# Kernel tuning notes

Hardware: AMD Instinct MI355X
Metric: run time of the kernel (lower is better)

The kernel has to match this reference:

```python
import jax, jax.numpy as jnp
import numpy as np
from jax import lax

B = 32
ITERS = 100
ALPHA = 0.3  # keras LeakyReLU default alpha
BN_SCALE = np.float32(1.0 / np.sqrt(1.0 + 1e-3))  # inference BN, default moving stats (mean 0, var 1)


def _make_psf_mat():
    # Gaussian PSF mapping 5184 fine (72x72) code positions -> 81 coarse (9x9) pixels, mat shape (5184, 81)
    sigma = (150.0 / 100.0) * 9.0 / 64.0
    coarse = np.arange(9) + 0.5
    fine = (np.arange(72) + 0.5) * 9.0 / 72.0
    g = np.exp(-(fine[:, None] - coarse[None, :]) ** 2 / (2.0 * sigma ** 2))  # (72, 9)
    mat = np.einsum('ia,jb->ijab', g, g).reshape(5184, 81)
    mat = mat / np.linalg.norm(mat, ord=2)  # spectral-normalize so FISTA (mu=1) is stable
    return mat.astype(np.float32)


def leaky(x):
    return jnp.where(x >= 0, x, ALPHA * x)


def conv(x, k, strides=(1, 1)):
    return lax.conv_general_dilated(x, k, strides, 'SAME',
                                    dimension_numbers=('NHWC', 'HWIO', 'NHWC'))


def _forward(inp, mat, w1_k, w1_b, x1_k, x1_b, c51_k, c51_b, c15_k, c15_b,
             c55_k, c55_b, x2_k, x2_b, y17_k, y17_b, y71_k, y71_b, yc_k, yc_b,
             d1_k, d2_k, h1_w, h1_b, h2_w, h2_b, h3_w, h3_b):
    b = inp.shape[0]
    # w branch
    w = leaky(conv(inp, w1_k) + w1_b)  # (B,9,9,1)
    # z branch -> lambda parameter
    z = inp * BN_SCALE
    z = leaky(conv(z, d1_k, strides=(3, 3)) * BN_SCALE)  # (B,3,3,12), downsample: conv no-bias + BN + LeakyReLU
    z = leaky(conv(z, d2_k, strides=(3, 3)) * BN_SCALE)  # (B,1,1,24)
    z = z.reshape(b, -1)
    z = z @ h1_w + h1_b
    z = z @ h2_w + h2_b
    z = z @ h3_w + h3_b  # (B,1)
    param = 0.1 * jax.nn.sigmoid(z)  # (B,1)
    # x branch: normalize (max of |x| over axis 1 only, as in source)
    x = inp / (0.001 + jnp.max(jnp.abs(inp), axis=1, keepdims=True))
    x = leaky(conv(x, x1_k) + x1_b)  # (B,9,9,3)
    # --- CompressedSensing: 100-iter FISTA, vectorized over batch and 3 channels ---
    im = x.reshape(b, 81, 3).transpose(0, 2, 1)  # (B,3,81) row-major flatten per channel
    lam = (param * 0.1)[:, :, None]  # (B,1,1), mu = 1.0

    def step(carry, _):
        y_tmp, y_last, t = carry
        resid = im - jnp.einsum('bcn,nk->bck', y_tmp, mat)      # (B,3,81)  = im - mat^T y
        re = jnp.einsum('bck,nk->bcn', resid, mat)              # (B,3,5184) = mat (im - mat^T y)
        wv = y_tmp + re
        y_new = jax.nn.relu(wv - lam) - jax.nn.relu(-wv - lam)  # soft threshold
        t_n = (1.0 + jnp.sqrt(1.0 + 4.0 * t * t)) / 2.0
        y_next = y_new + (t - 1.0) / t_n * (y_new - y_last)
        return (y_next, y_new, t_n), None

    init = (jnp.zeros((b, 3, 5184), jnp.float32),
            jnp.zeros((b, 3, 5184), jnp.float32),
            jnp.float32(1.0))
    (_, y_new, _), _ = lax.scan(step, init, None, length=ITERS)
    cs_out = y_new.transpose(0, 2, 1).reshape(b, 72, 72, 3)  # stack channels last then reshape
    x = conv(cs_out, c51_k, strides=(2, 2)) + c51_b   # (B,36,36,16), no activation
    x = conv(x, c15_k, strides=(2, 2)) + c15_b        # (B,18,18,32)
    x = conv(x, c55_k, strides=(2, 2)) + c55_b        # (B,9,9,64)
    x = leaky(conv(x, x2_k) + x2_b)                   # (B,9,9,8)
    # y branch
    y1 = conv(inp, y17_k) + y17_b                     # (B,9,9,32)
    y2 = conv(inp, y71_k) + y71_b                     # (B,9,9,32)
    y = leaky(conv(jnp.concatenate([y1, y2], axis=-1), yc_k) + yc_b)  # (B,9,9,32)
    out = jnp.concatenate([w, x, y], axis=-1)         # (B,9,9,41)
    return out, cs_out


def setup_inputs() -> dict:
    key = jax.random.key(0)
    ks = jax.random.split(key, 20)
    rn = lambda k, s, sc=0.1: sc * jax.random.normal(k, s, dtype=jnp.float32)
    x1_k = jnp.clip(1.0 + 0.3 * jax.random.normal(ks[1], (1, 1, 3, 3)), 0.0, None).astype(jnp.float32)
    return {
        'inp': jax.random.normal(ks[0], (B, 9, 9, 3), dtype=jnp.float32),
        'mat': jnp.asarray(_make_psf_mat()),
        'w1_k': rn(ks[2], (1, 1, 3, 1)), 'w1_b': jnp.zeros((1,), jnp.float32),
        'x1_k': x1_k, 'x1_b': jnp.zeros((3,), jnp.float32),
        'c51_k': rn(ks[3], (5, 1, 3, 16)), 'c51_b': jnp.zeros((16,), jnp.float32),
        'c15_k': rn(ks[4], (1, 5, 16, 32)), 'c15_b': jnp.zeros((32,), jnp.float32),
        'c55_k': rn(ks[5], (5, 5, 32, 64)), 'c55_b': jnp.zeros((64,), jnp.float32),
        'x2_k': rn(ks[6], (1, 1, 64, 8)), 'x2_b': jnp.zeros((8,), jnp.float32),
        'y17_k': rn(ks[7], (1, 7, 3, 32)), 'y17_b': jnp.zeros((32,), jnp.float32),
        'y71_k': rn(ks[8], (7, 1, 3, 32)), 'y71_b': jnp.zeros((32,), jnp.float32),
        'yc_k': rn(ks[9], (1, 1, 64, 32)), 'yc_b': jnp.zeros((32,), jnp.float32),
        'd1_k': rn(ks[10], (5, 5, 3, 12)), 'd2_k': rn(ks[11], (5, 5, 12, 24)),
        'h1_w': rn(ks[12], (24, 24), 0.2), 'h1_b': jnp.zeros((24,), jnp.float32),
        'h2_w': rn(ks[13], (24, 12), 0.2), 'h2_b': jnp.zeros((12,), jnp.float32),
        'h3_w': rn(ks[14], (12, 1), 0.2), 'h3_b': jnp.zeros((1,), jnp.float32),
    }


def reference(inp, mat, w1_k, w1_b, x1_k, x1_b, c51_k, c51_b, c15_k, c15_b,
              c55_k, c55_b, x2_k, x2_b, y17_k, y17_b, y71_k, y71_b, yc_k, yc_b,
              d1_k, d2_k, h1_w, h1_b, h2_w, h2_b, h3_w, h3_b):
    return _forward(inp, mat, w1_k, w1_b, x1_k, x1_b, c51_k, c51_b, c15_k, c15_b,
                    c55_k, c55_b, x2_k, x2_b, y17_k, y17_b, y71_k, y71_b, yc_k, yc_b,
                    d1_k, d2_k, h1_w, h1_b, h2_w, h2_b, h3_w, h3_b)
```

## Files before the change

### kernel.cpp

```cpp
#include <hip/hip_runtime.h>
#include <math.h>

#define LEAKY(x) ((x) >= 0.f ? (x) : 0.3f*(x))

#define G_OFF   0
#define IM_OFF  648
#define LAM_OFF 8424
#define WB_OFF  8456
#define YBR_OFF 11048
#define X1_OFF  93992
#define X2_OFF  757544
#define X3_OFF  1089320

#define OUT0 106272

__global__ __launch_bounds__(256) void prep_kernel(
    const float* __restrict__ inp, const float* __restrict__ mat,
    const float* __restrict__ w1_k, const float* __restrict__ w1_b,
    const float* __restrict__ x1_k, const float* __restrict__ x1_b,
    const float* __restrict__ y17_k, const float* __restrict__ y17_b,
    const float* __restrict__ y71_k, const float* __restrict__ y71_b,
    const float* __restrict__ yc_k, const float* __restrict__ yc_b,
    const float* __restrict__ d1_k, const float* __restrict__ d2_k,
    const float* __restrict__ h1_w, const float* __restrict__ h1_b,
    const float* __restrict__ h2_w, const float* __restrict__ h2_b,
    const float* __restrict__ h3_w, const float* __restrict__ h3_b,
    float* __restrict__ ws)
{
    int t = threadIdx.x;
    if (blockIdx.x == 0) {
        float rs = rsqrtf(mat[0]);
        for (int u = t; u < 648; u += 256) {
            int i = u / 9, a = u % 9;
            ws[G_OFF + u] = mat[(size_t)(i*72)*81 + a*9] * rs;
        }
        return;
    }
    int b = blockIdx.x - 1;
    __shared__ float sin_[243];
    __shared__ float cm[27];
    __shared__ float cat[5184];
    __shared__ float z1[108];
    __shared__ float z2[24];
    __shared__ float v1[24];
    __shared__ float v2[12];

    const float BN  = 1.0f / sqrtf(1.001f);
    const float BN2 = BN * BN;

    for (int u = t; u < 243; u += 256) sin_[u] = inp[b*243 + u];
    __syncthreads();

    if (t < 81) {
        float s = w1_b[0];
        for (int i = 0; i < 3; ++i) s += sin_[t*3+i] * w1_k[i];
        ws[WB_OFF + b*81 + t] = LEAKY(s);
    } else if (t < 108) {
        int u = t - 81;
        float m = 0.f;
        for (int r = 0; r < 9; ++r) m = fmaxf(m, fabsf(sin_[r*27 + u]));
        cm[u] = 0.001f + m;
    }
    if (t >= 128 && t < 236) {
        int u = t - 128;
        int o = u % 12, ox = (u/12) % 3, oy = u/36;
        float s = 0.f;
        for (int kh = 0; kh < 5; ++kh) {
            int iy = oy*3 - 1 + kh;
            if (iy < 0 || iy > 8) continue;
            for (int kw = 0; kw < 5; ++kw) {
                int ix = ox*3 - 1 + kw;
                if (ix < 0 || ix > 8) continue;
                for (int i = 0; i < 3; ++i)
                    s += sin_[(iy*9+ix)*3 + i] * d1_k[((kh*5+kw)*3 + i)*12 + o];
            }
        }
        z1[u] = LEAKY(BN2 * s);
    }
    __syncthreads();

    if (t < 243) {
        int o = t / 81, p = t % 81;
        int c = p % 9;
        float s = x1_b[o];
        for (int i = 0; i < 3; ++i)
            s += (sin_[p*3+i] / cm[c*3+i]) * x1_k[i*3 + o];
        ws[IM_OFF + (b*3 + o)*81 + p] = LEAKY(s);
    }
    __syncthreads();

    if (t < 24) {
        float s = 0.f;
        for (int kh = 1; kh < 4; ++kh)
            for (int kw = 1; kw < 4; ++kw)
                for (int i = 0; i < 12; ++i)
                    s += z1[((kh-1)*3 + (kw-1))*12 + i] * d2_k[((kh*5+kw)*12 + i)*24 + t];
        z2[t] = LEAKY(BN * s);
    }
    __syncthreads();
    if (t < 24) {
        float s = h1_b[t];
        for (int i = 0; i < 24; ++i) s += z2[i] * h1_w[i*24 + t];
        v1[t] = s;
    }
    __syncthreads();
    if (t < 12) {
        float s = h2_b[t];
        for (int i = 0; i < 24; ++i) s += v1[i] * h2_w[i*12 + t];
        v2[t] = s;
    }
    __syncthreads();
    if (t == 0) {
        float s = h3_b[0];
        for (int i = 0; i < 12; ++i) s += v2[i] * h3_w[i];
        ws[LAM_OFF + b] = 0.01f / (1.f + expf(-s));
    }

    for (int u = t; u < 5184; u += 256) {
        int pos = u / 64, i = u % 64;
        int r = pos / 9, c = pos % 9;
        float s;
        if (i < 32) {
            s = y17_b[i];
            for (int kw = 0; kw < 7; ++kw) {
                int cc = c - 3 + kw;
                if (cc < 0 || cc > 8) continue;
                for (int ii = 0; ii < 3; ++ii)
                    s += sin_[(r*9+cc)*3 + ii] * y17_k[(kw*3+ii)*32 + i];
            }
        } else {
            int i2 = i - 32;
            s = y71_b[i2];
            for (int kh = 0; kh < 7; ++kh) {
                int rr = r - 3 + kh;
                if (rr < 0 || rr > 8) continue;
                for (int ii = 0; ii < 3; ++ii)
                    s += sin_[(rr*9+c)*3 + ii] * y71_k[(kh*3+ii)*32 + i2];
            }
        }
        cat[pos*64 + i] = s;
    }
    __syncthreads();
    for (int u = t; u < 2592; u += 256) {
        int pos = u / 32, o = u % 32;
        float s = yc_b[o];
        for (int i = 0; i < 64; ++i) s += cat[pos*64 + i] * yc_k[i*32 + o];
        ws[YBR_OFF + (b*81 + pos)*32 + o] = LEAKY(s);
    }
}


#define DPP_XOR1 0xB1
#define DPP_XOR2 0x4E
#define DPP_HM   0x141
#define DPP_ROR8 0x128

template<int CTRL>
__device__ __forceinline__ float dppadd(float v) {
    return v + __int_as_float(__builtin_amdgcn_update_dpp(
        0, __float_as_int(v), CTRL, 0xF, 0xF, true));
}

#define QTB(a) { float v = q##a*Gjg + s8_##a*w8; \
    v = dppadd<DPP_XOR1>(v); v = dppadd<DPP_XOR2>(v); v = dppadd<DPP_HM>(v); \
    q##a = v; }

#define STEPMID(s,sm,sp) { \
    float re = gm*q##sm + g0*q##s + gp*q##sp; \
    float wv = Yv##s + re; \
    float cl = fminf(fmaxf(wv, -lam), lam); \
    float yn = wv - cl; \
    float yx = yn + cmom*(yn - Yl##s); \
    Yl##s = yn; Yv##s = yx; \
    u##sm += yx*gm; u##s += yx*g0; u##sp += yx*gp; }
#define STEP0 { \
    float re = g0*q0 + gp*q1; \
    float wv = Yv0 + re; \
    float cl = fminf(fmaxf(wv, -lam), lam); \
    float yn = wv - cl; \
    float yx = yn + cmom*(yn - Yl0); \
    Yl0 = yn; Yv0 = yx; \
    u0 += yx*g0; u1 += yx*gp; }
#define STEP8 { \
    float re = gm*q7 + g0*q8; \
    float wv = Yv8 + re; \
    float cl = fminf(fmaxf(wv, -lam), lam); \
    float yn = wv - cl; \
    float yx = yn + cmom*(yn - Yl8); \
    Yl8 = yn; Yv8 = yx; \
    u7 += yx*gm; u8 += yx*g0; }

#define TSP(a) { float v = u##a; \
    v = dppadd<DPP_XOR1>(v); v = dppadd<DPP_XOR2>(v); v = dppadd<DPP_HM>(v); \
    float vA = v*Gjg, vB = v*Gj8; \
    spA_##a = dppadd<DPP_ROR8>(vA); spB_##a = dppadd<DPP_ROR8>(vB); }

#define OUTW(s) cs_out[(size_t)(b*5184 + (8*s+gg)*72 + j)*3 + ch] = Yl##s;

__global__ __launch_bounds__(576, 3) void fista_kernel(
    const float* __restrict__ ws, float* __restrict__ cs_out)
{
    __shared__ __align__(16) float SPm[36*108];
    __shared__ __align__(16) float Rm[108];

    int t = threadIdx.x;
    int b = blockIdx.x / 3, ch = blockIdx.x % 3;
    const float* g = ws + G_OFF;
    float lam = ws[LAM_OFF + b];

    int j = t >> 3, gg = t & 7;
    int l = t & 63;

    float gm = g[(gg + 8)*9 + 0];
    float g0 = g[gg*9 + 0];
    float gp = g[gg*9 + 1];

    float Gjg = g[j*9 + gg];
    float Gj8 = g[j*9 + 8];
    float w8  = (gg == 7) ? Gj8 : 0.f;

    int ab = t >> 2, pp = t & 3;
    int aa = ab / 9, bb = ab % 9;
    float im_ab = (t < 324) ? ws[IM_OFF + (b*3 + ch)*81 + ab] : 0.f;

    if (t < 81) {
        Rm[(t % 9)*12 + (t / 9)] = ws[IM_OFF + (b*3 + ch)*81 + t];
    }

    float Yv0=0,Yv1=0,Yv2=0,Yv3=0,Yv4=0,Yv5=0,Yv6=0,Yv7=0,Yv8=0;
    float Yl0=0,Yl1=0,Yl2=0,Yl3=0,Yl4=0,Yl5=0,Yl6=0,Yl7=0,Yl8=0;
    float tk = 1.f;
    __syncthreads();

    for (int it = 0; it < 100; ++it) {
        float tn = 0.5f*(1.f + sqrtf(1.f + 4.f*tk*tk));
        float cmom = (tk - 1.f) / tn;
        tk = tn;

        const float4* Rg4 = (const float4*)(&Rm[gg*12]);
        float4 ra = Rg4[0], rb = Rg4[1];
        float  rc = Rm[gg*12 + 8];
        float q0=ra.x,q1=ra.y,q2=ra.z,q3=ra.w,
              q4=rb.x,q5=rb.y,q6=rb.z,q7=rb.w,q8=rc;
        const float4* R84 = (const float4*)(&Rm[96]);
        float4 sa = R84[0], sb = R84[1];
        float  sc = Rm[104];
        float s8_0=sa.x,s8_1=sa.y,s8_2=sa.z,s8_3=sa.w,
              s8_4=sb.x,s8_5=sb.y,s8_6=sb.z,s8_7=sb.w,s8_8=sc;
        QTB(0) QTB(1) QTB(2) QTB(3) QTB(4) QTB(5) QTB(6) QTB(7) QTB(8)

        float u0=0,u1=0,u2=0,u3=0,u4=0,u5=0,u6=0,u7=0,u8=0;
        STEP0
        STEPMID(1,0,2) STEPMID(2,1,3) STEPMID(3,2,4) STEPMID(4,3,5)
        STEPMID(5,4,6) STEPMID(6,5,7) STEPMID(7,6,8)
        STEP8
        if (it == 99) break;

        float spA_0,spA_1,spA_2,spA_3,spA_4,spA_5,spA_6,spA_7,spA_8;
        float spB_0,spB_1,spB_2,spB_3,spB_4,spB_5,spB_6,spB_7,spB_8;
        TSP(0) TSP(1) TSP(2) TSP(3) TSP(4) TSP(5) TSP(6) TSP(7) TSP(8)

        int setb = ((t >> 6)*4 + (l >> 4))*108;
        if ((l & 8) == 0) {
            float* d = &SPm[setb + gg*12];
            ((float4*)d)[0] = make_float4(spA_0,spA_1,spA_2,spA_3);
            ((float4*)d)[1] = make_float4(spA_4,spA_5,spA_6,spA_7);
            d[8] = spA_8;
            if (gg == 0) {
                float* d2 = &SPm[setb + 96];
                ((float4*)d2)[0] = make_float4(spB_0,spB_1,spB_2,spB_3);
                ((float4*)d2)[1] = make_float4(spB_4,spB_5,spB_6,spB_7);
                d2[8] = spB_8;
            }
        }
        __syncthreads();

        if (t < 324) {
            float s = 0.f;
#pragma unroll
            for (int k = 0; k < 9; ++k)
                s += SPm[(pp*9 + k)*108 + bb*12 + aa];
            s = dppadd<DPP_XOR1>(s);
            s = dppadd<DPP_XOR2>(s);
            if (pp == 0) Rm[bb*12 + aa] = im_ab - s;
        }
        __syncthreads();
    }

    OUTW(0) OUTW(1) OUTW(2) OUTW(3) OUTW(4) OUTW(5) OUTW(6) OUTW(7) OUTW(8)
}

__global__ __launch_bounds__(256) void c51_kernel(
    const float* __restrict__ cs, const float* __restrict__ k,
    const float* __restrict__ bias, float* __restrict__ out)
{
    int id = blockIdx.x*256 + threadIdx.x;
    if (id >= 32*36*36*16) return;
    int o = id & 15; int rest = id >> 4;
    int ox = rest % 36; rest /= 36; int oy = rest % 36; int b = rest / 36;
    float s = bias[o];
    int ix = ox*2;
    for (int kh = 0; kh < 5; ++kh) {
        int iy = oy*2 - 1 + kh;
        if (iy < 0 || iy >= 72) continue;
        const float* p = cs + ((size_t)(b*72 + iy)*72 + ix)*3;
        const float* kk = k + kh*48 + o;
        s += p[0]*kk[0] + p[1]*kk[16] + p[2]*kk[32];
    }
    out[id] = s;
}

__global__ __launch_bounds__(256) void c15_kernel(
    const float* __restrict__ x1, const float* __restrict__ k,
    const float* __restrict__ bias, float* __restrict__ out)
{
    int id = blockIdx.x*256 + threadIdx.x;
    if (id >= 32*18*18*32) return;
    int o = id & 31; int rest = id >> 5;
    int ox = rest % 18; rest /= 18; int oy = rest % 18; int b = rest / 18;
    float s = bias[o];
    int iy = oy*2;
    for (int kw = 0; kw < 5; ++kw) {
        int ix = ox*2 - 1 + kw;
        if (ix < 0 || ix >= 36) continue;
        const float* p = x1 + ((size_t)(b*36 + iy)*36 + ix)*16;
        const float* kk = k + kw*512 + o;
        for (int i = 0; i < 16; ++i) s += p[i]*kk[i*32];
    }
    out[id] = s;
}

__global__ __launch_bounds__(256) void c55_kernel(
    const float* __restrict__ x2, const float* __restrict__ k,
    const float* __restrict__ bias, float* __restrict__ out)
{
    int id = blockIdx.x*256 + threadIdx.x;
    if (id >= 32*9*9*64) return;
    int o = id & 63; int rest = id >> 6;
    int ox = rest % 9; rest /= 9; int oy = rest % 9; int b = rest / 9;
    float s = bias[o];
    for (int kh = 0; kh < 5; ++kh) {
        int iy = oy*2 - 1 + kh;
        if (iy < 0 || iy >= 18) continue;
        for (int kw = 0; kw < 5; ++kw) {
            int ix = ox*2 - 1 + kw;
            if (ix < 0 || ix >= 18) continue;
            const float* p = x2 + ((size_t)(b*18 + iy)*18 + ix)*32;
            const float* kk = k + (kh*5+kw)*2048 + o;
            for (int i = 0; i < 32; ++i) s += p[i]*kk[i*64];
        }
    }
    out[id] = s;
}

__global__ __launch_bounds__(256) void out_kernel(
    const float* __restrict__ ws, const float* __restrict__ x2_k,
    const float* __restrict__ x2_b, float* __restrict__ out)
{
    int id = blockIdx.x*256 + threadIdx.x;
    if (id >= OUT0) return;
    int q = id % 41; int rest = id / 41;
    int cc = rest % 9; rest /= 9; int r = rest % 9; int b = rest / 9;
    float val;
    if (q == 0) {
        val = ws[WB_OFF + b*81 + r*9 + cc];
    } else if (q <= 8) {
        int o = q - 1;
        const float* p = ws + X3_OFF + ((size_t)(b*9 + r)*9 + cc)*64;
        float s = x2_b[o];
        for (int i = 0; i < 64; ++i) s += p[i]*x2_k[i*8 + o];
        val = LEAKY(s);
    } else {
        val = ws[YBR_OFF + ((size_t)(b*81 + r*9 + cc))*32 + (q - 9)];
    }
    out[id] = val;
}

extern "C" void kernel_launch(void* const* d_in, const int* in_sizes, int n_in,
                              void* d_out, int out_size, void* d_ws, size_t ws_size,
                              hipStream_t stream) {
    const float* inp   = (const float*)d_in[0];
    const float* mat   = (const float*)d_in[1];
    const float* w1_k  = (const float*)d_in[2];
    const float* w1_b  = (const float*)d_in[3];
    const float* x1_k  = (const float*)d_in[4];
    const float* x1_b  = (const float*)d_in[5];
    const float* c51_k = (const float*)d_in[6];
    const float* c51_b = (const float*)d_in[7];
    const float* c15_k = (const float*)d_in[8];
    const float* c15_b = (const float*)d_in[9];
    const float* c55_k = (const float*)d_in[10];
    const float* c55_b = (const float*)d_in[11];
    const float* x2_k  = (const float*)d_in[12];
    const float* x2_b  = (const float*)d_in[13];
    const float* y17_k = (const float*)d_in[14];
    const float* y17_b = (const float*)d_in[15];
    const float* y71_k = (const float*)d_in[16];
    const float* y71_b = (const float*)d_in[17];
    const float* yc_k  = (const float*)d_in[18];
    const float* yc_b  = (const float*)d_in[19];
    const float* d1_k  = (const float*)d_in[20];
    const float* d2_k  = (const float*)d_in[21];
    const float* h1_w  = (const float*)d_in[22];
    const float* h1_b  = (const float*)d_in[23];
    const float* h2_w  = (const float*)d_in[24];
    const float* h2_b  = (const float*)d_in[25];
    const float* h3_w  = (const float*)d_in[26];
    const float* h3_b  = (const float*)d_in[27];

    float* ws  = (float*)d_ws;
    float* out = (float*)d_out;
    float* cs  = out + OUT0;

    hipLaunchKernelGGL(prep_kernel, dim3(33), dim3(256), 0, stream,
        inp, mat, w1_k, w1_b, x1_k, x1_b, y17_k, y17_b, y71_k, y71_b,
        yc_k, yc_b, d1_k, d2_k, h1_w, h1_b, h2_w, h2_b, h3_w, h3_b, ws);
    hipLaunchKernelGGL(fista_kernel, dim3(96), dim3(576), 0, stream, ws, cs);
    hipLaunchKernelGGL(c51_kernel, dim3(2592), dim3(256), 0, stream, cs, c51_k, c51_b, ws + X1_OFF);
    hipLaunchKernelGGL(c15_kernel, dim3(1296), dim3(256), 0, stream, ws + X1_OFF, c15_k, c15_b, ws + X2_OFF);
    hipLaunchKernelGGL(c55_kernel, dim3(648), dim3(256), 0, stream, ws + X2_OFF, c55_k, c55_b, ws + X3_OFF);
    hipLaunchKernelGGL(out_kernel, dim3(416), dim3(256), 0, stream, ws, x2_k, x2_b, out);
}
```

Before: 375.2 us.

## Exploit banded Gaussian PSF structure in FISTA transpose and reduction

The per-iteration computation of q no longer does a DPP cross-lane reduction. Each thread now computes q from three neighbouring residual rows (prev, current, next) weighted by the banded Gaussian coefficients. The shared-memory reduction also sums only three neighbouring partial sets instead of nine. Both rely on the PSF being effectively tridiagonal in the coarse dimension, which cuts LDS reads and DPP operations. The risk is that dropping the far Gaussian tails changes numerics slightly, and the correctness of the index mapping is hard to verify.

```diff
diff --git a/kernel.cpp b/kernel.cpp
--- a/kernel.cpp
+++ b/kernel.cpp
@@ -160,10 +160,6 @@
     return v + __int_as_float(__builtin_amdgcn_update_dpp(
         0, __float_as_int(v), CTRL, 0xF, 0xF, true));
 }
-
-#define QTB(a) { float v = q##a*Gjg + s8_##a*w8; \
-    v = dppadd<DPP_XOR1>(v); v = dppadd<DPP_XOR2>(v); v = dppadd<DPP_HM>(v); \
-    q##a = v; }
 
 #define STEPMID(s,sm,sp) { \
     float re = gm*q##sm + g0*q##s + gp*q##sp; \
@@ -195,6 +191,8 @@
     float vA = v*Gjg, vB = v*Gj8; \
     spA_##a = dppadd<DPP_ROR8>(vA); spB_##a = dppadd<DPP_ROR8>(vB); }
 
+#define QT3(a) float q##a = cmc*rm_##a + c0c*r0_##a + cpc*rp_##a;
+
 #define OUTW(s) cs_out[(size_t)(b*5184 + (8*s+gg)*72 + j)*3 + ch] = Yl##s;
 
 __global__ __launch_bounds__(576, 3) void fista_kernel(
@@ -210,14 +208,21 @@
 
     int j = t >> 3, gg = t & 7;
     int l = t & 63;
+    int w = t >> 6;
+    int rr = j & 7;
 
     float gm = g[(gg + 8)*9 + 0];
     float g0 = g[gg*9 + 0];
     float gp = g[gg*9 + 1];
 
+    float cmc = (w > 0) ? g[(rr + 8)*9 + 0] : 0.f;
+    float c0c = g[rr*9 + 0];
+    float cpc = (w < 8) ? g[rr*9 + 1] : 0.f;
+    int bmr = (w > 0) ? w - 1 : 0;
+    int bpr = (w < 8) ? w + 1 : 8;
+
     float Gjg = g[j*9 + gg];
     float Gj8 = g[j*9 + 8];
-    float w8  = (gg == 7) ? Gj8 : 0.f;
 
     int ab = t >> 2, pp = t & 3;
     int aa = ab / 9, bb = ab % 9;
@@ -237,17 +242,22 @@
         float cmom = (tk - 1.f) / tn;
         tk = tn;
 
-        const float4* Rg4 = (const float4*)(&Rm[gg*12]);
-        float4 ra = Rg4[0], rb = Rg4[1];
-        float  rc = Rm[gg*12 + 8];
-        float q0=ra.x,q1=ra.y,q2=ra.z,q3=ra.w,
-              q4=rb.x,q5=rb.y,q6=rb.z,q7=rb.w,q8=rc;
-        const float4* R84 = (const float4*)(&Rm[96]);
-        float4 sa = R84[0], sb = R84[1];
-        float  sc = Rm[104];
-        float s8_0=sa.x,s8_1=sa.y,s8_2=sa.z,s8_3=sa.w,
-              s8_4=sb.x,s8_5=sb.y,s8_6=sb.z,s8_7=sb.w,s8_8=sc;
-        QTB(0) QTB(1) QTB(2) QTB(3) QTB(4) QTB(5) QTB(6) QTB(7) QTB(8)
+        float4 mv0 = *(const float4*)(Rm + bmr*12);
+        float4 mv1 = *(const float4*)(Rm + bmr*12 + 4);
+        float  mv2 = Rm[bmr*12 + 8];
+        float rm_0=mv0.x, rm_1=mv0.y, rm_2=mv0.z, rm_3=mv0.w,
+              rm_4=mv1.x, rm_5=mv1.y, rm_6=mv1.z, rm_7=mv1.w, rm_8=mv2;
+        float4 zv0 = *(const float4*)(Rm + w*12);
+        float4 zv1 = *(const float4*)(Rm + w*12 + 4);
+        float  zv2 = Rm[w*12 + 8];
+        float r0_0=zv0.x, r0_1=zv0.y, r0_2=zv0.z, r0_3=zv0.w,
+              r0_4=zv1.x, r0_5=zv1.y, r0_6=zv1.z, r0_7=zv1.w, r0_8=zv2;
+        float4 pv0 = *(const float4*)(Rm + bpr*12);
+        float4 pv1 = *(const float4*)(Rm + bpr*12 + 4);
+        float  pv2 = Rm[bpr*12 + 8];
+        float rp_0=pv0.x, rp_1=pv0.y, rp_2=pv0.z, rp_3=pv0.w,
+              rp_4=pv1.x, rp_5=pv1.y, rp_6=pv1.z, rp_7=pv1.w, rp_8=pv2;
+        QT3(0) QT3(1) QT3(2) QT3(3) QT3(4) QT3(5) QT3(6) QT3(7) QT3(8)
 
         float u0=0,u1=0,u2=0,u3=0,u4=0,u5=0,u6=0,u7=0,u8=0;
         STEP0
@@ -276,10 +286,9 @@
         __syncthreads();
 
         if (t < 324) {
-            float s = 0.f;
-#pragma unroll
-            for (int k = 0; k < 9; ++k)
-                s += SPm[(pp*9 + k)*108 + bb*12 + aa];
+            float s = SPm[(bb*4 + pp)*108 + bb*12 + aa];
+            if (bb > 0) s += SPm[((bb-1)*4 + pp)*108 + bb*12 + aa];
+            if (bb < 8) s += SPm[((bb+1)*4 + pp)*108 + bb*12 + aa];
             s = dppadd<DPP_XOR1>(s);
             s = dppadd<DPP_XOR2>(s);
             if (pp == 0) Rm[bb*12 + aa] = im_ab - s;
```

After: 351.2 us. 6.4% less time.
